# Performance work log

Hardware: AMD Instinct MI355X
Metric: run time of the kernel (lower is better)

## Reference

```python
import jax, jax.numpy as jnp
import numpy as np

B = 8
SHAPE = (4, 16, 16)   # latent video shape; S = prod = 1024
S = 1024
AE = 64               # ae_embed_dim
D = 768               # embed_dim
F = 3072              # mlp_dim
H = 12                # num_heads (heads are re-merged before the score matmul!)
L = 12                # num_layers
C = 17                # n_classes
OUT = 1024            # out_dim
EPS = 1e-6
HD = D // H


def setup_inputs() -> dict:
    key = jax.random.key(0)
    ks = iter(jax.random.split(key, 64))

    def p(shape, s=0.02):
        return jax.random.normal(next(ks), shape, jnp.float32) * s

    inp = {
        'x': jax.random.normal(next(ks), (B, *SHAPE, AE), jnp.float32),
        'mask': jnp.tril(jnp.ones((S, S), bool)),  # causal
        'label': jax.nn.one_hot(jax.random.randint(next(ks), (B,), 0, C), C, dtype=jnp.float32),
        'dense_in_w': p((D, AE)), 'dense_in_b': jnp.zeros((D,), jnp.float32),
        'sos': p((D,)),
        # BroadcastPositionBiases: embed_dim=768 split into 3 chunks of 256
        'pos0': p((SHAPE[0], D // 3)), 'pos1': p((SHAPE[1], D // 3)), 'pos2': p((SHAPE[2], D // 3)),
        'ln1_sw': p((L, D, C)), 'ln1_bw': p((L, D, C)),
        'qkv_w': p((L, 3 * D, D)), 'qkv_b': jnp.zeros((L, 3 * D), jnp.float32),
        'ao1_w': p((L, D, D)), 'ao1_b': jnp.zeros((L, D), jnp.float32),  # DotProductAttention.out_proj
        'ao2_w': p((L, D, D)), 'ao2_b': jnp.zeros((L, D), jnp.float32),  # MultiHeadAttention.out_proj
        'ln2_sw': p((L, D, C)), 'ln2_bw': p((L, D, C)),
        'mlp_w1': p((L, F, D)), 'mlp_b1': jnp.zeros((L, F), jnp.float32),
        'mlp_w2': p((L, D, F)), 'mlp_b2': jnp.zeros((L, D), jnp.float32),
        'lnf_sw': p((D, C)), 'lnf_bw': p((D, C)),
        'out_w': p((OUT, D)), 'out_b': jnp.zeros((OUT,), jnp.float32),
    }
    return inp


def cond_ln(x, cond, sw, bw):
    # conditional LayerNorm: mul = rsqrt(var+eps)*(1+Linear(cond)), bias = Linear(cond)
    mean = jnp.mean(x, axis=-1, keepdims=True)
    var = jnp.mean((x - mean) ** 2, axis=-1, keepdims=True)
    scale = cond @ sw.T   # [B, D]
    bias = cond @ bw.T    # [B, D]
    mul = jax.lax.rsqrt(var + EPS) * (1.0 + scale[:, None, :])
    return (x - mean) * mul + bias[:, None, :]


def pos_bias(embs, shape):
    n = len(shape)
    outs = []
    for i, e in enumerate(embs):
        sh = [1] * n + [e.shape[-1]]
        sh[i] = shape[i]
        outs.append(jnp.broadcast_to(e.reshape(sh), tuple(shape) + (e.shape[-1],)))
    return jnp.concatenate(outs, axis=-1).reshape(-1, sum(e.shape[-1] for e in embs))  # [S, D]


def attn_block(h, mask, qkv_w, qkv_b, o1_w, o1_b, o2_w, o2_b):
    Bn, Sn, Dn = h.shape
    qkv = h @ qkv_w.T + qkv_b                       # [B, S, 3D]
    qkv = qkv.reshape(Bn, Sn, H, 3 * HD)            # per-head [q|k|v] layout
    q = qkv[..., :HD].reshape(Bn, Sn, Dn)           # heads re-merged BEFORE scores
    k = qkv[..., HD:2 * HD].reshape(Bn, Sn, Dn)
    v = qkv[..., 2 * HD:].reshape(Bn, Sn, Dn)
    # NOTE: scaling uses full embed_dim (module quirk), not head_dim
    scores = jnp.einsum('bqd,bkd->bqk', q * (float(Dn) ** -0.5), k)
    scores = jnp.where(mask[None, :, :], scores, -jnp.inf)
    w = jax.nn.softmax(scores, axis=-1)
    out = jnp.einsum('bqk,bkd->bqd', w, v)
    out = out @ o1_w.T + o1_b                        # DotProductAttention.out_proj
    out = out @ o2_w.T + o2_b                        # MultiHeadAttention.out_proj (applied twice)
    return out


def _forward(x, mask, label, dense_in_w, dense_in_b, sos, pos0, pos1, pos2,
             ln1_sw, ln1_bw, qkv_w, qkv_b, ao1_w, ao1_b, ao2_w, ao2_b,
             ln2_sw, ln2_bw, mlp_w1, mlp_b1, mlp_w2, mlp_b2,
             lnf_sw, lnf_bw, out_w, out_b):
    Bn = x.shape[0]
    old_shape = x.shape[1:-1]
    h = x.reshape(Bn, -1, x.shape[-1]) @ dense_in_w.T + dense_in_b   # [B, S, D]
    # right shift with learned SOS token
    h = jnp.concatenate([jnp.broadcast_to(sos, (Bn, 1, D)), h[:, :-1]], axis=1)
    pb = pos_bias([pos0, pos1, pos2], old_shape)                     # [S, D]
    h = h + pb[None, :h.shape[1]]
    for l in range(L):
        hn = cond_ln(h, label, ln1_sw[l], ln1_bw[l])
        h = h + attn_block(hn, mask, qkv_w[l], qkv_b[l], ao1_w[l], ao1_b[l], ao2_w[l], ao2_b[l])
        hn = cond_ln(h, label, ln2_sw[l], ln2_bw[l])
        m = hn @ mlp_w1[l].T + mlp_b1[l]
        m = jax.nn.sigmoid(1.702 * m) * m           # GELU2
        m = m @ mlp_w2[l].T + mlp_b2[l]
        h = h + m
    h = cond_ln(h, label, lnf_sw, lnf_bw)
    out = h @ out_w.T + out_b                        # [B, S, OUT]
    return out.reshape(Bn, *old_shape, out.shape[-1])


def reference(x, mask, label, dense_in_w, dense_in_b, sos, pos0, pos1, pos2,
              ln1_sw, ln1_bw, qkv_w, qkv_b, ao1_w, ao1_b, ao2_w, ao2_b,
              ln2_sw, ln2_bw, mlp_w1, mlp_b1, mlp_w2, mlp_b2,
              lnf_sw, lnf_bw, out_w, out_b):
    return _forward(x, mask, label, dense_in_w, dense_in_b, sos, pos0, pos1, pos2,
                    ln1_sw, ln1_bw, qkv_w, qkv_b, ao1_w, ao1_b, ao2_w, ao2_b,
                    ln2_sw, ln2_bw, mlp_w1, mlp_b1, mlp_w2, mlp_b2,
                    lnf_sw, lnf_bw, out_w, out_b)
```

## Files before the change

### kernel.cpp

```cpp
#include <hip/hip_runtime.h>

typedef __bf16 bf16;
typedef __bf16 bf16x8 __attribute__((ext_vector_type(8)));
typedef __bf16 bf16x4 __attribute__((ext_vector_type(4)));
typedef float  f32x4  __attribute__((ext_vector_type(4)));

#define DEV __device__ __forceinline__

DEV void gload_lds16(const bf16* g, bf16* l) {
    __builtin_amdgcn_global_load_lds(
        (__attribute__((address_space(1))) void*)g,
        (__attribute__((address_space(3))) void*)l, 16, 0, 0);
}

DEV void barrier_raw() {
    asm volatile("" ::: "memory");
    __builtin_amdgcn_s_barrier();
    asm volatile("" ::: "memory");
}

enum { M_QKV, M_SCORES, M_PV, M_RESID, M_GELU, M_OUT, M_WM };

template<int MODE>
__global__ __launch_bounds__(256)
void gemm_k(const bf16* __restrict__ A, const bf16* __restrict__ B,
            int M, int N, int K,
            long long batchA, long long batchB, long long batchC,
            const float* __restrict__ bias,
            bf16* __restrict__ Cb, float* __restrict__ Cf,
            bf16* __restrict__ qp, bf16* __restrict__ kp, bf16* __restrict__ vp)
{
    const int bm = blockIdx.x, bn = blockIdx.y, bz = blockIdx.z;
    const int kTiles = K >> 5;

    const int tid = threadIdx.x, wid = tid >> 6, lane = tid & 63;
    const bf16* Ab = A + (long long)bz * batchA + (long long)bm * 128 * K;
    const bf16* Bb = B + (long long)bz * batchB + (long long)bn * 128 * K;

    extern __shared__ __align__(16) bf16 smem[];
    bf16* sA = smem;
    bf16* sB = smem + 16384;

    const int srow = wid * 16 + (lane >> 2);
    const int scol = (lane & 3) * 8;
    const long long aoff = (long long)srow * K + scol;

    auto stage = [&](int buf, int kt) {
        const bf16* ga = Ab + (long long)kt * 32;
        const bf16* gb = Bb + (long long)kt * 32;
        bf16* a = sA + buf * 4096;
        bf16* b = sB + buf * 4096;
        gload_lds16(ga + aoff,            a + (wid * 16) * 32);
        gload_lds16(ga + aoff + 64LL * K, a + (64 + wid * 16) * 32);
        gload_lds16(gb + aoff,            b + (wid * 16) * 32);
        gload_lds16(gb + aoff + 64LL * K, b + (64 + wid * 16) * 32);
    };

    f32x4 acc[4][4];
#pragma unroll
    for (int m = 0; m < 4; ++m)
#pragma unroll
        for (int n = 0; n < 4; ++n) acc[m][n] = (f32x4){0.f, 0.f, 0.f, 0.f};

    const int npre = kTiles < 3 ? kTiles : 3;
    for (int t = 0; t < npre; ++t) stage(t, t);

    const int wr = wid >> 1, wc = wid & 1;
    const int arow = wr * 64 + (lane & 15);
    const int brow = wc * 64 + (lane & 15);
    const int koff = (lane >> 4) * 8;

    for (int kt = 0; kt < kTiles; ++kt) {
        const int rem = kTiles - 1 - kt;
        if (rem >= 2)      asm volatile("s_waitcnt vmcnt(8)" ::: "memory");
        else if (rem == 1) asm volatile("s_waitcnt vmcnt(4)" ::: "memory");
        else               asm volatile("s_waitcnt vmcnt(0)" ::: "memory");
        barrier_raw();
        if (kt + 3 < kTiles) stage((kt + 3) & 3, kt + 3);

        const int cur = kt & 3;
        const bf16* a = sA + cur * 4096;
        const bf16* b = sB + cur * 4096;
        bf16x8 af[4], bfr[4];
#pragma unroll
        for (int m = 0; m < 4; ++m)
            af[m] = *(const bf16x8*)&a[(arow + m * 16) * 32 + koff];
#pragma unroll
        for (int n = 0; n < 4; ++n)
            bfr[n] = *(const bf16x8*)&b[(brow + n * 16) * 32 + koff];
#pragma unroll
        for (int m = 0; m < 4; ++m)
#pragma unroll
            for (int n = 0; n < 4; ++n)
                acc[m][n] = __builtin_amdgcn_mfma_f32_16x16x32_bf16(af[m], bfr[n], acc[m][n], 0, 0, 0);
    }

    const int cr0 = bm * 128 + wr * 64 + (lane >> 4) * 4;
    const int cc0 = bn * 128 + wc * 64 + (lane & 15);
#pragma unroll
    for (int m = 0; m < 4; ++m) {
#pragma unroll
        for (int n = 0; n < 4; ++n) {
            const int col = cc0 + n * 16;
#pragma unroll
            for (int r = 0; r < 4; ++r) {
                const int row = cr0 + m * 16 + r;
                float v = acc[m][n][r];
                if (MODE == M_QKV) {
                    v += bias[col];
                    int hd = col / 192, rr = col % 192;
                    int b2 = row >> 10, s = row & 1023;
                    if (rr < 64)
                        qp[(long long)row * 768 + hd * 64 + rr] = (bf16)(v * 0.03608439182435161f);
                    else if (rr < 128)
                        kp[(long long)row * 768 + hd * 64 + (rr - 64)] = (bf16)v;
                    else
                        vp[((long long)b2 * 768 + hd * 64 + (rr - 128)) * 1024 + s] = (bf16)v;
                } else if (MODE == M_GELU) {
                    float xg = v + bias[col];
                    Cb[(long long)row * N + col] = (bf16)(xg / (1.f + __expf(-1.702f * xg)));
                } else if (MODE == M_RESID) {
                    long long idx = (long long)row * N + col;
                    Cf[idx] += v + bias[col];
                } else if (MODE == M_WM) {
                    Cb[(long long)bz * batchC + (long long)row * N + col] = (bf16)v;
                } else {
                    Cf[(long long)row * N + col] = v + bias[col];
                }
            }
        }
    }
}

template<int MODE>
__global__ __launch_bounds__(256)
void gemm64_k(const bf16* __restrict__ A, const bf16* __restrict__ B,
              int M, int N, int K,
              long long batchA, long long batchB, long long batchC,
              const float* __restrict__ bias,
              bf16* __restrict__ Cb, float* __restrict__ Cf)
{
    const int bm = blockIdx.x, bn = blockIdx.y, bz = blockIdx.z;
    if (MODE == M_SCORES && 2 * bn > bm) return;
    int kTiles = K >> 5;
    if (MODE == M_PV) {
        int lim = 2 * bm + 2;
        if (lim < kTiles) kTiles = lim;
    }

    const int tid = threadIdx.x, wid = tid >> 6, lane = tid & 63;
    const bf16* Ab = A + (long long)bz * batchA + (long long)bm * 64 * K;
    const bf16* Bb = B + (long long)bz * batchB + (long long)bn * 128 * K;

    extern __shared__ __align__(16) bf16 smem[];
    bf16* sA = smem;
    bf16* sB = smem + 8192;

    const int srow = wid * 16 + (lane >> 2);
    const int scol = (lane & 3) * 8;
    const long long aoff = (long long)srow * K + scol;

    auto stage = [&](int buf, int kt) {
        const bf16* ga = Ab + (long long)kt * 32;
        const bf16* gb = Bb + (long long)kt * 32;
        gload_lds16(ga + aoff,            sA + buf * 2048 + (wid * 16) * 32);
        gload_lds16(gb + aoff,            sB + buf * 4096 + (wid * 16) * 32);
        gload_lds16(gb + aoff + 64LL * K, sB + buf * 4096 + (64 + wid * 16) * 32);
    };

    f32x4 acc[2][4];
#pragma unroll
    for (int m = 0; m < 2; ++m)
#pragma unroll
        for (int n = 0; n < 4; ++n) acc[m][n] = (f32x4){0.f, 0.f, 0.f, 0.f};

    const int npre = kTiles < 3 ? kTiles : 3;
    for (int t = 0; t < npre; ++t) stage(t, t);

    const int wr = wid >> 1, wc = wid & 1;
    const int arow = wr * 32 + (lane & 15);
    const int brow = wc * 64 + (lane & 15);
    const int koff = (lane >> 4) * 8;

    for (int kt = 0; kt < kTiles; ++kt) {
        const int rem = kTiles - 1 - kt;
        if (rem >= 2)      asm volatile("s_waitcnt vmcnt(6)" ::: "memory");
        else if (rem == 1) asm volatile("s_waitcnt vmcnt(3)" ::: "memory");
        else               asm volatile("s_waitcnt vmcnt(0)" ::: "memory");
        barrier_raw();
        if (kt + 3 < kTiles) stage((kt + 3) & 3, kt + 3);

        const int cur = kt & 3;
        const bf16* a = sA + cur * 2048;
        const bf16* b = sB + cur * 4096;
        bf16x8 af[2], bfr[4];
#pragma unroll
        for (int m = 0; m < 2; ++m)
            af[m] = *(const bf16x8*)&a[(arow + m * 16) * 32 + koff];
#pragma unroll
        for (int n = 0; n < 4; ++n)
            bfr[n] = *(const bf16x8*)&b[(brow + n * 16) * 32 + koff];
#pragma unroll
        for (int m = 0; m < 2; ++m)
#pragma unroll
            for (int n = 0; n < 4; ++n)
                acc[m][n] = __builtin_amdgcn_mfma_f32_16x16x32_bf16(af[m], bfr[n], acc[m][n], 0, 0, 0);
    }

    const int cr0 = bm * 64 + wr * 32 + (lane >> 4) * 4;
    const int cc0 = bn * 128 + wc * 64 + (lane & 15);
#pragma unroll
    for (int m = 0; m < 2; ++m) {
#pragma unroll
        for (int n = 0; n < 4; ++n) {
            const int col = cc0 + n * 16;
#pragma unroll
            for (int r = 0; r < 4; ++r) {
                const int row = cr0 + m * 16 + r;
                float v = acc[m][n][r];
                if (MODE == M_SCORES || MODE == M_PV) {
                    Cb[(long long)bz * batchC + (long long)row * N + col] = (bf16)v;
                } else {
                    Cf[(long long)row * N + col] = v + bias[col];
                }
            }
        }
    }
}

__global__ __launch_bounds__(256)
void cvt_bf16_k(const float* __restrict__ in, bf16* __restrict__ out, int n4)
{
    int i = blockIdx.x * 256 + threadIdx.x;
    if (i >= n4) return;
    float4 f = ((const float4*)in)[i];
    bf16x4 o = { (bf16)f.x, (bf16)f.y, (bf16)f.z, (bf16)f.w };
    ((bf16x4*)out)[i] = o;
}

__global__ __launch_bounds__(256)
void transpose_cvt_k(const float* __restrict__ in, bf16* __restrict__ out, int n)
{
    __shared__ float t[32][33];
    const int l = blockIdx.z;
    const int r0 = blockIdx.y * 32, c0 = blockIdx.x * 32;
    const float* src = in + (long long)l * n * n;
    bf16* dst = out + (long long)l * n * n;
    const int tx = threadIdx.x & 31, ty = threadIdx.x >> 5;
#pragma unroll
    for (int i = 0; i < 32; i += 8)
        t[ty + i][tx] = src[(long long)(r0 + ty + i) * n + c0 + tx];
    __syncthreads();
#pragma unroll
    for (int i = 0; i < 32; i += 8)
        dst[(long long)(c0 + ty + i) * n + r0 + tx] = (bf16)t[tx][ty + i];
}

__global__ __launch_bounds__(256)
void bias_merge_k(const float* __restrict__ o2w, const float* __restrict__ o1b,
                  const float* __restrict__ o2b, float* __restrict__ bm, int total)
{
    const int wid = threadIdx.x >> 6, lane = threadIdx.x & 63;
    const int idx = blockIdx.x * 4 + wid;
    if (idx >= total) return;
    const int l = idx / 768, a = idx - l * 768;
    const float* wrow = o2w + ((long long)l * 768 + a) * 768;
    const float* brow = o1b + (long long)l * 768;
    float s = 0.f;
#pragma unroll
    for (int j = 0; j < 12; ++j) {
        int c = j * 64 + lane;
        s += wrow[c] * brow[c];
    }
#pragma unroll
    for (int o = 32; o; o >>= 1) s += __shfl_down(s, o);
    if (lane == 0) bm[idx] = s + o2b[(long long)l * 768 + a];
}

__global__ __launch_bounds__(256)
void cond_proj_k(const float* __restrict__ label, const float* __restrict__ sw,
                 const float* __restrict__ bw, float* __restrict__ scale,
                 float* __restrict__ bias, int total)
{
    int idx = blockIdx.x * 256 + threadIdx.x;
    if (idx >= total) return;
    int l = idx / 6144;
    int rem = idx - l * 6144;
    int b = rem / 768, d = rem - (rem / 768) * 768;
    const float* lab = label + b * 17;
    const float* swp = sw + ((long long)l * 768 + d) * 17;
    const float* bwp = bw + ((long long)l * 768 + d) * 17;
    float s = 0.f, bb = 0.f;
#pragma unroll
    for (int c = 0; c < 17; ++c) { float lv = lab[c]; s += lv * swp[c]; bb += lv * bwp[c]; }
    scale[idx] = s;
    bias[idx]  = bb;
}

__global__ __launch_bounds__(256)
void shift_pos_k(const float* __restrict__ xe, const float* __restrict__ sos,
                 const float* __restrict__ p0, const float* __restrict__ p1,
                 const float* __restrict__ p2, float* __restrict__ h)
{
    const int s = blockIdx.x, b = blockIdx.y;
    const int i0 = s >> 8, i1 = (s >> 4) & 15, i2 = s & 15;
    const float* xr = xe + ((long long)b * 1024 + (s - 1)) * 768;
#pragma unroll
    for (int j = 0; j < 3; ++j) {
        const int d = j * 256 + threadIdx.x;
        float v = (s == 0) ? sos[d] : xr[d];
        float pbv = (d < 256) ? p0[i0 * 256 + d]
                  : (d < 512) ? p1[i1 * 256 + (d - 256)]
                              : p2[i2 * 256 + (d - 512)];
        h[((long long)b * 1024 + s) * 768 + d] = v + pbv;
    }
}

__global__ __launch_bounds__(256)
void cond_ln_k(const float* __restrict__ h, const float* __restrict__ scale,
               const float* __restrict__ bias, bf16* __restrict__ out)
{
    const long long row = (long long)blockIdx.y * 1024 + blockIdx.x;
    const int b = blockIdx.y;
    const float* hr = h + row * 768;
    float v[3], sum = 0.f, sq = 0.f;
#pragma unroll
    for (int j = 0; j < 3; ++j) {
        v[j] = hr[j * 256 + threadIdx.x];
        sum += v[j]; sq += v[j] * v[j];
    }
    __shared__ float sm[8];
#pragma unroll
    for (int o = 32; o; o >>= 1) { sum += __shfl_down(sum, o); sq += __shfl_down(sq, o); }
    const int wid = threadIdx.x >> 6;
    if ((threadIdx.x & 63) == 0) { sm[wid] = sum; sm[4 + wid] = sq; }
    __syncthreads();
    sum = sm[0] + sm[1] + sm[2] + sm[3];
    sq  = sm[4] + sm[5] + sm[6] + sm[7];
    const float mean = sum * (1.f / 768.f);
    const float var  = sq * (1.f / 768.f) - mean * mean;
    const float rs   = rsqrtf(var + 1e-6f);
    const float* sc = scale + (long long)b * 768;
    const float* bi = bias  + (long long)b * 768;
    bf16* orow = out + row * 768;
#pragma unroll
    for (int j = 0; j < 3; ++j) {
        const int d = j * 256 + threadIdx.x;
        orow[d] = (bf16)((v[j] - mean) * rs * (1.f + sc[d]) + bi[d]);
    }
}

__global__ __launch_bounds__(256)
void softmax_k(bf16* __restrict__ P)
{
    const int i = blockIdx.x, b = blockIdx.y;
    bf16* row = P + ((long long)b * 1024 + i) * 1024;
    const int len = i + 1;
    const int lim = (i | 63) + 1;
    float v[4], mx = -1e30f;
#pragma unroll
    for (int j = 0; j < 4; ++j) {
        int c = j * 256 + threadIdx.x;
        v[j] = (c < len) ? (float)row[c] : -1e30f;
        mx = fmaxf(mx, v[j]);
    }
    __shared__ float sm[8];
#pragma unroll
    for (int o = 32; o; o >>= 1) mx = fmaxf(mx, __shfl_down(mx, o));
    const int wid = threadIdx.x >> 6;
    if ((threadIdx.x & 63) == 0) sm[wid] = mx;
    __syncthreads();
    mx = fmaxf(fmaxf(sm[0], sm[1]), fmaxf(sm[2], sm[3]));
    float s = 0.f;
#pragma unroll
    for (int j = 0; j < 4; ++j) {
        v[j] = __expf(v[j] - mx);
        s += ((j * 256 + threadIdx.x) < len) ? v[j] : 0.f;
    }
#pragma unroll
    for (int o = 32; o; o >>= 1) s += __shfl_down(s, o);
    if ((threadIdx.x & 63) == 0) sm[4 + wid] = s;
    __syncthreads();
    s = sm[4] + sm[5] + sm[6] + sm[7];
    const float inv = 1.f / s;
#pragma unroll
    for (int j = 0; j < 4; ++j) {
        int c = j * 256 + threadIdx.x;
        if (c < lim) row[c] = (c < len) ? (bf16)(v[j] * inv) : (bf16)0.f;
    }
}

__global__ __launch_bounds__(256)
void fill_k(float* o, int n, float v)
{
    int i = blockIdx.x * 256 + threadIdx.x;
    if (i < n) o[i] = v;
}

extern "C" void kernel_launch(void* const* d_in, const int* in_sizes, int n_in,
                              void* d_out, int out_size, void* d_ws, size_t ws_size,
                              hipStream_t stream)
{
    (void)in_sizes; (void)n_in;
    const float* x     = (const float*)d_in[0];
    const float* label = (const float*)d_in[2];
    const float* dw    = (const float*)d_in[3];
    const float* db    = (const float*)d_in[4];
    const float* sos   = (const float*)d_in[5];
    const float* p0    = (const float*)d_in[6];
    const float* p1    = (const float*)d_in[7];
    const float* p2    = (const float*)d_in[8];
    const float* ln1sw = (const float*)d_in[9];
    const float* ln1bw = (const float*)d_in[10];
    const float* qkvw  = (const float*)d_in[11];
    const float* qkvb  = (const float*)d_in[12];
    const float* ao1w  = (const float*)d_in[13];
    const float* ao1b  = (const float*)d_in[14];
    const float* ao2w  = (const float*)d_in[15];
    const float* ao2b  = (const float*)d_in[16];
    const float* ln2sw = (const float*)d_in[17];
    const float* ln2bw = (const float*)d_in[18];
    const float* m1w   = (const float*)d_in[19];
    const float* m1b   = (const float*)d_in[20];
    const float* m2w   = (const float*)d_in[21];
    const float* m2b   = (const float*)d_in[22];
    const float* lnfsw = (const float*)d_in[23];
    const float* lnfbw = (const float*)d_in[24];
    const float* outw  = (const float*)d_in[25];
    const float* outb  = (const float*)d_in[26];
    float* out = (float*)d_out;

    char* p = (char*)d_ws;
    auto alloc = [&](size_t bytes) { void* r = (void*)p; p += (bytes + 255) & ~(size_t)255; return r; };
    float* h    = (float*)alloc(8192LL * 768 * 4);
    bf16*  hn   = (bf16*) alloc(8192LL * 768 * 2);
    bf16*  q    = (bf16*) alloc(8192LL * 768 * 2);
    bf16*  kbuf = (bf16*) alloc(8192LL * 768 * 2);
    bf16*  vT   = (bf16*) alloc(8192LL * 768 * 2);
    bf16*  P    = (bf16*) alloc(8LL * 1024 * 1024 * 2);
    bf16*  attn = (bf16*) alloc(8192LL * 768 * 2);
    bf16*  mb   = (bf16*) alloc(8192LL * 3072 * 2);
    bf16*  wout = (bf16*) alloc(1024LL * 768 * 2);
    bf16*  wmA  = (bf16*) alloc(12LL * 768 * 768 * 2);
    float* bmA  = (float*)alloc(12LL * 768 * 4);
    float* s1   = (float*)alloc(12LL * 8 * 768 * 4);
    float* b1   = (float*)alloc(12LL * 8 * 768 * 4);
    float* s2   = (float*)alloc(12LL * 8 * 768 * 4);
    float* b2   = (float*)alloc(12LL * 8 * 768 * 4);
    float* sf   = (float*)alloc(8LL * 768 * 4);
    float* bfb  = (float*)alloc(8LL * 768 * 4);

    size_t base_needed = (size_t)(p - (char*)d_ws);
    if (base_needed + 16LL * 1024 * 1024 > ws_size) {
        fill_k<<<(out_size + 255) / 256, 256, 0, stream>>>(out, out_size, 1e9f);
        return;
    }

    const long long SZ_QKV = 2304LL * 768, SZ_O = 768LL * 768, SZ_M = 3072LL * 768;
    size_t all_bytes = (size_t)(12 * (SZ_QKV + 2 * SZ_M)) * 2;
    bool allw = ((size_t)(p - (char*)d_ws) + all_bytes + 4096 <= ws_size);

    bf16 *wqkvA, *wm1A, *wm2A;
    if (allw) {
        wqkvA = (bf16*)alloc(12 * SZ_QKV * 2);
        wm1A  = (bf16*)alloc(12 * SZ_M * 2);
        wm2A  = (bf16*)alloc(12 * SZ_M * 2);
    } else {
        wqkvA = (bf16*)alloc(SZ_QKV * 2);
        wm1A  = (bf16*)alloc(SZ_M * 2);
        wm2A  = (bf16*)alloc(SZ_M * 2);
    }

    bf16*  xbf   = (bf16*)P;
    bf16*  dwbf  = (bf16*)P + 524288;
    bf16*  wo2bf = (bf16*)P + 1048576;
    float* xe    = (float*)mb;
    bf16*  o1t   = mb + 12582912;

    cvt_bf16_k<<<1024 * 768 / 4 / 256, 256, 0, stream>>>(outw, wout, 1024 * 768 / 4);
    cond_proj_k<<<(12 * 8 * 768 + 255) / 256, 256, 0, stream>>>(label, ln1sw, ln1bw, s1, b1, 12 * 8 * 768);
    cond_proj_k<<<(12 * 8 * 768 + 255) / 256, 256, 0, stream>>>(label, ln2sw, ln2bw, s2, b2, 12 * 8 * 768);
    cond_proj_k<<<(8 * 768 + 255) / 256, 256, 0, stream>>>(label, lnfsw, lnfbw, sf, bfb, 8 * 768);

    if (allw) {
        cvt_bf16_k<<<(int)(12 * SZ_QKV / 4 / 256), 256, 0, stream>>>(qkvw, wqkvA, (int)(12 * SZ_QKV / 4));
        cvt_bf16_k<<<(int)(12 * SZ_M / 4 / 256),   256, 0, stream>>>(m1w,  wm1A,  (int)(12 * SZ_M / 4));
        cvt_bf16_k<<<(int)(12 * SZ_M / 4 / 256),   256, 0, stream>>>(m2w,  wm2A,  (int)(12 * SZ_M / 4));
    }

    cvt_bf16_k<<<(int)(12 * SZ_O / 4 / 256), 256, 0, stream>>>(ao2w, wo2bf, (int)(12 * SZ_O / 4));
    transpose_cvt_k<<<dim3(24, 24, 12), 256, 0, stream>>>(ao1w, o1t, 768);
    gemm_k<M_WM><<<dim3(6, 6, 12), 256, 65536, stream>>>(
        wo2bf, o1t, 768, 768, 768, SZ_O, SZ_O, SZ_O,
        nullptr, wmA, nullptr, nullptr, nullptr, nullptr);
    bias_merge_k<<<(12 * 768 + 3) / 4, 256, 0, stream>>>(ao2w, ao1b, ao2b, bmA, 12 * 768);

    cvt_bf16_k<<<8192 * 64 / 4 / 256, 256, 0, stream>>>(x, xbf, 8192 * 64 / 4);
    cvt_bf16_k<<<768 * 64 / 4 / 256, 256, 0, stream>>>(dw, dwbf, 768 * 64 / 4);
    gemm_k<M_OUT><<<dim3(64, 6, 1), 256, 65536, stream>>>(
        xbf, dwbf, 8192, 768, 64, 0, 0, 0, db, nullptr, xe, nullptr, nullptr, nullptr);
    shift_pos_k<<<dim3(1024, 8), 256, 0, stream>>>(xe, sos, p0, p1, p2, h);

    for (int l = 0; l < 12; ++l) {
        bf16 *wqkv, *wm1, *wm2;
        if (allw) {
            wqkv = wqkvA + (long long)l * SZ_QKV;
            wm1  = wm1A  + (long long)l * SZ_M;
            wm2  = wm2A  + (long long)l * SZ_M;
        } else {
            wqkv = wqkvA; wm1 = wm1A; wm2 = wm2A;
            cvt_bf16_k<<<(int)(SZ_QKV / 4 / 256), 256, 0, stream>>>(qkvw + (long long)l * SZ_QKV, wqkv, (int)(SZ_QKV / 4));
            cvt_bf16_k<<<(int)(SZ_M / 4 / 256),   256, 0, stream>>>(m1w  + (long long)l * SZ_M,   wm1,  (int)(SZ_M / 4));
            cvt_bf16_k<<<(int)(SZ_M / 4 / 256),   256, 0, stream>>>(m2w  + (long long)l * SZ_M,   wm2,  (int)(SZ_M / 4));
        }

        cond_ln_k<<<dim3(1024, 8), 256, 0, stream>>>(h, s1 + (long long)l * 6144, b1 + (long long)l * 6144, hn);

        gemm_k<M_QKV><<<dim3(64, 18, 1), 256, 65536, stream>>>(
            hn, wqkv, 8192, 2304, 768, 0, 0, 0,
            qkvb + (long long)l * 2304, nullptr, nullptr, q, kbuf, vT);

        gemm64_k<M_SCORES><<<dim3(16, 8, 8), 256, 49152, stream>>>(
            q, kbuf, 1024, 1024, 768, 1024LL * 768, 1024LL * 768, 1024LL * 1024,
            nullptr, P, nullptr);

        softmax_k<<<dim3(1024, 8), 256, 0, stream>>>(P);

        gemm64_k<M_PV><<<dim3(16, 6, 8), 256, 49152, stream>>>(
            P, vT, 1024, 768, 1024, 1024LL * 1024, 768LL * 1024, 1024LL * 768,
            nullptr, attn, nullptr);

        gemm_k<M_RESID><<<dim3(64, 6, 1), 256, 65536, stream>>>(
            attn, wmA + (long long)l * SZ_O, 8192, 768, 768, 0, 0, 0,
            bmA + (long long)l * 768, nullptr, h, nullptr, nullptr, nullptr);

        cond_ln_k<<<dim3(1024, 8), 256, 0, stream>>>(h, s2 + (long long)l * 6144, b2 + (long long)l * 6144, hn);

        gemm_k<M_GELU><<<dim3(64, 24, 1), 256, 65536, stream>>>(
            hn, wm1, 8192, 3072, 768, 0, 0, 0,
            m1b + (long long)l * 3072, mb, nullptr, nullptr, nullptr, nullptr);

        gemm_k<M_RESID><<<dim3(64, 6, 1), 256, 65536, stream>>>(
            mb, wm2, 8192, 768, 3072, 0, 0, 0,
            m2b + (long long)l * 768, nullptr, h, nullptr, nullptr, nullptr);
    }

    cond_ln_k<<<dim3(1024, 8), 256, 0, stream>>>(h, sf, bfb, hn);
    gemm64_k<M_OUT><<<dim3(128, 8, 1), 256, 49152, stream>>>(
        hn, wout, 8192, 1024, 768, 0, 0, 0,
        outb, nullptr, out);
}
```

Before: 3.980 ms.

## Use triple-buffered LDS pipeline and 64-row tiles for residual GEMMs

Both GEMM kernels drop from four LDS stages to three, with prefetch depth two and a rotating buffer index, cutting shared memory per block (64KB to 48KB, 48KB to 36KB) so more blocks can be resident per CU. The two residual-add GEMMs (attention out-projection and MLP down-projection, N=768) now use the 64-row tile kernel with a new accumulate epilogue, doubling the grid to 768 blocks for better CU fill. The trade-off is less latency hiding from the shallower prefetch and lower per-block data reuse in the residual GEMMs.

```diff
diff --git a/kernel.cpp b/kernel.cpp
--- a/kernel.cpp
+++ b/kernel.cpp
@@ -39,7 +39,7 @@
 
     extern __shared__ __align__(16) bf16 smem[];
     bf16* sA = smem;
-    bf16* sB = smem + 16384;
+    bf16* sB = smem + 12288;
 
     const int srow = wid * 16 + (lane >> 2);
     const int scol = (lane & 3) * 8;
@@ -62,7 +62,7 @@
 #pragma unroll
         for (int n = 0; n < 4; ++n) acc[m][n] = (f32x4){0.f, 0.f, 0.f, 0.f};
 
-    const int npre = kTiles < 3 ? kTiles : 3;
+    const int npre = kTiles < 2 ? kTiles : 2;
     for (int t = 0; t < npre; ++t) stage(t, t);
 
     const int wr = wid >> 1, wc = wid & 1;
@@ -70,15 +70,16 @@
     const int brow = wc * 64 + (lane & 15);
     const int koff = (lane >> 4) * 8;
 
+    int cur = 0;
     for (int kt = 0; kt < kTiles; ++kt) {
-        const int rem = kTiles - 1 - kt;
-        if (rem >= 2)      asm volatile("s_waitcnt vmcnt(8)" ::: "memory");
-        else if (rem == 1) asm volatile("s_waitcnt vmcnt(4)" ::: "memory");
-        else               asm volatile("s_waitcnt vmcnt(0)" ::: "memory");
+        if (kt + 1 < kTiles) asm volatile("s_waitcnt vmcnt(4)" ::: "memory");
+        else                 asm volatile("s_waitcnt vmcnt(0)" ::: "memory");
         barrier_raw();
-        if (kt + 3 < kTiles) stage((kt + 3) & 3, kt + 3);
-
-        const int cur = kt & 3;
+        if (kt + 2 < kTiles) {
+            int ib = cur - 1; if (ib < 0) ib = 2;
+            stage(ib, kt + 2);
+        }
+
         const bf16* a = sA + cur * 4096;
         const bf16* b = sB + cur * 4096;
         bf16x8 af[4], bfr[4];
@@ -93,6 +94,8 @@
 #pragma unroll
             for (int n = 0; n < 4; ++n)
                 acc[m][n] = __builtin_amdgcn_mfma_f32_16x16x32_bf16(af[m], bfr[n], acc[m][n], 0, 0, 0);
+
+        cur = (cur == 2) ? 0 : cur + 1;
     }
 
     const int cr0 = bm * 128 + wr * 64 + (lane >> 4) * 4;
@@ -154,7 +157,7 @@
 
     extern __shared__ __align__(16) bf16 smem[];
     bf16* sA = smem;
-    bf16* sB = smem + 8192;
+    bf16* sB = smem + 6144;
 
     const int srow = wid * 16 + (lane >> 2);
     const int scol = (lane & 3) * 8;
@@ -174,7 +177,7 @@
 #pragma unroll
         for (int n = 0; n < 4; ++n) acc[m][n] = (f32x4){0.f, 0.f, 0.f, 0.f};
 
-    const int npre = kTiles < 3 ? kTiles : 3;
+    const int npre = kTiles < 2 ? kTiles : 2;
     for (int t = 0; t < npre; ++t) stage(t, t);
 
     const int wr = wid >> 1, wc = wid & 1;
@@ -182,15 +185,16 @@
     const int brow = wc * 64 + (lane & 15);
     const int koff = (lane >> 4) * 8;
 
+    int cur = 0;
     for (int kt = 0; kt < kTiles; ++kt) {
-        const int rem = kTiles - 1 - kt;
-        if (rem >= 2)      asm volatile("s_waitcnt vmcnt(6)" ::: "memory");
-        else if (rem == 1) asm volatile("s_waitcnt vmcnt(3)" ::: "memory");
-        else               asm volatile("s_waitcnt vmcnt(0)" ::: "memory");
+        if (kt + 1 < kTiles) asm volatile("s_waitcnt vmcnt(3)" ::: "memory");
+        else                 asm volatile("s_waitcnt vmcnt(0)" ::: "memory");
         barrier_raw();
-        if (kt + 3 < kTiles) stage((kt + 3) & 3, kt + 3);
-
-        const int cur = kt & 3;
+        if (kt + 2 < kTiles) {
+            int ib = cur - 1; if (ib < 0) ib = 2;
+            stage(ib, kt + 2);
+        }
+
         const bf16* a = sA + cur * 2048;
         const bf16* b = sB + cur * 4096;
         bf16x8 af[2], bfr[4];
@@ -205,6 +209,8 @@
 #pragma unroll
             for (int n = 0; n < 4; ++n)
                 acc[m][n] = __builtin_amdgcn_mfma_f32_16x16x32_bf16(af[m], bfr[n], acc[m][n], 0, 0, 0);
+
+        cur = (cur == 2) ? 0 : cur + 1;
     }
 
     const int cr0 = bm * 64 + wr * 32 + (lane >> 4) * 4;
@@ -220,6 +226,9 @@
                 float v = acc[m][n][r];
                 if (MODE == M_SCORES || MODE == M_PV) {
                     Cb[(long long)bz * batchC + (long long)row * N + col] = (bf16)v;
+                } else if (MODE == M_RESID) {
+                    long long idx = (long long)row * N + col;
+                    Cf[idx] += v + bias[col];
                 } else {
                     Cf[(long long)row * N + col] = v + bias[col];
                 }
@@ -490,14 +499,14 @@
 
     cvt_bf16_k<<<(int)(12 * SZ_O / 4 / 256), 256, 0, stream>>>(ao2w, wo2bf, (int)(12 * SZ_O / 4));
     transpose_cvt_k<<<dim3(24, 24, 12), 256, 0, stream>>>(ao1w, o1t, 768);
-    gemm_k<M_WM><<<dim3(6, 6, 12), 256, 65536, stream>>>(
+    gemm_k<M_WM><<<dim3(6, 6, 12), 256, 49152, stream>>>(
         wo2bf, o1t, 768, 768, 768, SZ_O, SZ_O, SZ_O,
         nullptr, wmA, nullptr, nullptr, nullptr, nullptr);
     bias_merge_k<<<(12 * 768 + 3) / 4, 256, 0, stream>>>(ao2w, ao1b, ao2b, bmA, 12 * 768);
 
     cvt_bf16_k<<<8192 * 64 / 4 / 256, 256, 0, stream>>>(x, xbf, 8192 * 64 / 4);
     cvt_bf16_k<<<768 * 64 / 4 / 256, 256, 0, stream>>>(dw, dwbf, 768 * 64 / 4);
-    gemm_k<M_OUT><<<dim3(64, 6, 1), 256, 65536, stream>>>(
+    gemm_k<M_OUT><<<dim3(64, 6, 1), 256, 49152, stream>>>(
         xbf, dwbf, 8192, 768, 64, 0, 0, 0, db, nullptr, xe, nullptr, nullptr, nullptr);
     shift_pos_k<<<dim3(1024, 8), 256, 0, stream>>>(xe, sos, p0, p1, p2, h);
 
@@ -516,37 +525,37 @@
 
         cond_ln_k<<<dim3(1024, 8), 256, 0, stream>>>(h, s1 + (long long)l * 6144, b1 + (long long)l * 6144, hn);
 
-        gemm_k<M_QKV><<<dim3(64, 18, 1), 256, 65536, stream>>>(
+        gemm_k<M_QKV><<<dim3(64, 18, 1), 256, 49152, stream>>>(
             hn, wqkv, 8192, 2304, 768, 0, 0, 0,
             qkvb + (long long)l * 2304, nullptr, nullptr, q, kbuf, vT);
 
-        gemm64_k<M_SCORES><<<dim3(16, 8, 8), 256, 49152, stream>>>(
+        gemm64_k<M_SCORES><<<dim3(16, 8, 8), 256, 36864, stream>>>(
             q, kbuf, 1024, 1024, 768, 1024LL * 768, 1024LL * 768, 1024LL * 1024,
             nullptr, P, nullptr);
 
         softmax_k<<<dim3(1024, 8), 256, 0, stream>>>(P);
 
-        gemm64_k<M_PV><<<dim3(16, 6, 8), 256, 49152, stream>>>(
+        gemm64_k<M_PV><<<dim3(16, 6, 8), 256, 36864, stream>>>(
             P, vT, 1024, 768, 1024, 1024LL * 1024, 768LL * 1024, 1024LL * 768,
             nullptr, attn, nullptr);
 
-        gemm_k<M_RESID><<<dim3(64, 6, 1), 256, 65536, stream>>>(
+        gemm64_k<M_RESID><<<dim3(128, 6, 1), 256, 36864, stream>>>(
             attn, wmA + (long long)l * SZ_O, 8192, 768, 768, 0, 0, 0,
-            bmA + (long long)l * 768, nullptr, h, nullptr, nullptr, nullptr);
+            bmA + (long long)l * 768, nullptr, h);
 
         cond_ln_k<<<dim3(1024, 8), 256, 0, stream>>>(h, s2 + (long long)l * 6144, b2 + (long long)l * 6144, hn);
 
-        gemm_k<M_GELU><<<dim3(64, 24, 1), 256, 65536, stream>>>(
+        gemm_k<M_GELU><<<dim3(64, 24, 1), 256, 49152, stream>>>(
             hn, wm1, 8192, 3072, 768, 0, 0, 0,
             m1b + (long long)l * 3072, mb, nullptr, nullptr, nullptr, nullptr);
 
-        gemm_k<M_RESID><<<dim3(64, 6, 1), 256, 65536, stream>>>(
+        gemm64_k<M_RESID><<<dim3(128, 6, 1), 256, 36864, stream>>>(
             mb, wm2, 8192, 768, 3072, 0, 0, 0,
-            m2b + (long long)l * 768, nullptr, h, nullptr, nullptr, nullptr);
+            m2b + (long long)l * 768, nullptr, h);
     }
 
     cond_ln_k<<<dim3(1024, 8), 256, 0, stream>>>(h, sf, bfb, hn);
-    gemm64_k<M_OUT><<<dim3(128, 8, 1), 256, 49152, stream>>>(
+    gemm64_k<M_OUT><<<dim3(128, 8, 1), 256, 36864, stream>>>(
         hn, wout, 8192, 1024, 768, 0, 0, 0,
         outb, nullptr, out);
 }
```

Result: no change. 3.905 ms (-1.9%).
